# Performance work log

Hardware: AMD Instinct MI355X
Metric: run time of the kernel (lower is better)

Reference implementation:

```python
import jax, jax.numpy as jnp
import numpy as np


def setup_inputs() -> dict:
    key = jax.random.key(0)
    ks = jax.random.split(key, 4)
    B, S, D, E = 8, 4096, 2048, 64
    scale = 1.0 / np.sqrt(D)
    return {
        "x": jax.random.normal(ks[0], (B, S, D), dtype=jnp.float32),
        "W_route": jax.random.normal(ks[1], (E, D), dtype=jnp.float32) * scale,
        "b_route": jnp.zeros((E,), dtype=jnp.float32),
        "W_noise": jax.random.normal(ks[2], (E, D), dtype=jnp.float32) * scale,
        "b_noise": jnp.zeros((E,), dtype=jnp.float32),
        "noise_eps": jax.random.normal(ks[3], (B, S, E), dtype=jnp.float32),
    }


TOP_K = 2


def reference(x, W_route, b_route, W_noise, b_noise, noise_eps):
    # Dual linear projections: [B,S,D] @ [D,E] -> [B,S,E]
    logits = jnp.einsum("bsd,ed->bse", x, W_route) + b_route
    noise_logits = jnp.einsum("bsd,ed->bse", x, W_noise) + b_noise
    noisy_logits = logits + noise_eps * jax.nn.softplus(noise_logits)

    B, S, E = noisy_logits.shape
    flat = noisy_logits.reshape(B * S, E)
    top_vals, top_idx = jax.lax.top_k(flat, TOP_K)  # [N,K]

    # Scatter top-k values into -inf background, then softmax over experts.
    neg_inf = jnp.full_like(flat, -jnp.inf)
    rows = jnp.arange(B * S)[:, None]
    sparse = neg_inf.at[rows, top_idx].set(top_vals)
    router_output = jax.nn.softmax(sparse, axis=-1).reshape(B, S, E)
    indices = top_idx.reshape(B, S, TOP_K)
    return router_output, indices
```

## Files before the change

### kernel.cpp

```cpp
#include <hip/hip_runtime.h>
#include <math.h>

typedef _Float16 f16;
typedef __attribute__((ext_vector_type(8))) _Float16 half8;
typedef __attribute__((ext_vector_type(4))) float f32x4;

#define NEXP 64
#define TMR 32
#define TM 64
#define L_STRIDE 132

__device__ __forceinline__ float softplus_f(float x) {
    return fmaxf(x, 0.0f) + log1pf(expf(-fabsf(x)));
}

__device__ __forceinline__ void lds_dma16(const void* g, void* l) {
    __builtin_amdgcn_global_load_lds(
        (const __attribute__((address_space(1))) unsigned int*)g,
        (__attribute__((address_space(3))) unsigned int*)l, 16, 0, 0);
}

__device__ __forceinline__ void cvt_split(const float4 a, const float4 b,
                                          half8& hv, half8& lv) {
    const float vv[8] = {a.x, a.y, a.z, a.w, b.x, b.y, b.z, b.w};
#pragma unroll
    for (int j = 0; j < 8; ++j) {
        const f16 h = (f16)vv[j];
        hv[j] = h;
        lv[j] = (f16)((vv[j] - (float)h) * 4096.0f);
    }
}

__global__ void wsplit_kernel(const float* __restrict__ Wr,
                              const float* __restrict__ Wn,
                              f16* __restrict__ ws, int D) {
    const int per_col = D >> 3;
    const int t = blockIdx.x * blockDim.x + threadIdx.x;
    const int col = t / per_col;
    const int k0  = (t - col * per_col) * 8;
    if (col >= 128) return;
    const float* src = (col < NEXP) ? &Wr[(size_t)col * D] : &Wn[(size_t)(col - NEXP) * D];
    const float4 v0 = *(const float4*)&src[k0];
    const float4 v1 = *(const float4*)&src[k0 + 4];
    half8 hi, lo;
    cvt_split(v0, v1, hi, lo);
    const int kc = k0 >> 5, q = (k0 >> 3) & 3;
    const size_t base = (size_t)kc * 8192 + (size_t)q * 1024 + (size_t)col * 8;
    *(half8*)&ws[base]        = hi;
    *(half8*)&ws[base + 4096] = lo;
}

__global__ __launch_bounds__(256, 4)
void router_mfma_kernel(const float* __restrict__ x,
                        const f16* __restrict__ wsW,
                        const float* __restrict__ br,
                        const float* __restrict__ bn,
                        const float* __restrict__ eps,
                        float* __restrict__ out,
                        int N, int D) {
    __shared__ union alignas(16) {
        f16 B[2][8192];
        struct {
            float L[TMR][L_STRIDE];
            float p1[TMR], p2[TMR];
            int   i1[TMR], i2[TMR];
        } ep;
    } sm;

    const int tid  = threadIdx.x;
    const int lane = tid & 63;
    const int w    = tid >> 6;
    const int rowbase = blockIdx.x * TMR;
    const int wr = w & 1, wc = w >> 1;
    const int quad = lane >> 4;
    const int l16  = lane & 15;

    f32x4 accM[4], accC[4];
#pragma unroll
    for (int j = 0; j < 4; ++j) {
        accM[j] = (f32x4){0.f, 0.f, 0.f, 0.f};
        accC[j] = (f32x4){0.f, 0.f, 0.f, 0.f};
    }

    const float* xA = x + (size_t)(rowbase + wr * 16 + l16) * D + quad * 8;
    const int nkc = D >> 5;

    float4 aE0, aE1, aO0, aO1;

    {
        const char* gsrc = (const char*)wsW + w * 4096 + lane * 16;
        char* ldst = (char*)&sm.B[0][0] + w * 4096;
#pragma unroll
        for (int i = 0; i < 4; ++i) lds_dma16(gsrc + i * 1024, ldst + i * 1024);
        __builtin_amdgcn_sched_barrier(0);
        aE0 = *(const float4*)&xA[0];
        aE1 = *(const float4*)&xA[4];
        aO0 = *(const float4*)&xA[32];
        aO1 = *(const float4*)&xA[36];
        __builtin_amdgcn_sched_barrier(0);
        asm volatile("s_waitcnt vmcnt(4)" : : : "memory");
        __builtin_amdgcn_s_barrier();
        __builtin_amdgcn_sched_barrier(0);
    }

#define KLOOP_BODY(KC, A0, A1)                                                 \
    {                                                                          \
        const int cur = (KC) & 1, nxt = cur ^ 1;                               \
        if ((KC) + 1 < nkc) {                                                  \
            const char* gsrc = (const char*)wsW + (size_t)((KC) + 1) * 16384   \
                               + w * 4096 + lane * 16;                         \
            char* ldst = (char*)&sm.B[nxt][0] + w * 4096;                      \
            lds_dma16(gsrc,        ldst);                                      \
            lds_dma16(gsrc + 1024, ldst + 1024);                               \
            lds_dma16(gsrc + 2048, ldst + 2048);                               \
            lds_dma16(gsrc + 3072, ldst + 3072);                               \
        }                                                                      \
        __builtin_amdgcn_sched_barrier(0);                                     \
        half8 ah, al;                                                          \
        cvt_split(A0, A1, ah, al);                                             \
        if ((KC) + 2 < nkc) {                                                  \
            A0 = *(const float4*)&xA[((KC) + 2) * 32];                         \
            A1 = *(const float4*)&xA[((KC) + 2) * 32 + 4];                     \
        }                                                                      \
        __builtin_amdgcn_sched_barrier(0);                                     \
        half8 bh[4], bl[4];                                                    \
        _Pragma("unroll")                                                      \
        for (int ct = 0; ct < 4; ++ct) {                                       \
            const int c = (wc * 64 + ct * 16 + l16) * 8;                       \
            bh[ct] = *(const half8*)&sm.B[cur][quad * 1024 + c];               \
            bl[ct] = *(const half8*)&sm.B[cur][4096 + quad * 1024 + c];        \
        }                                                                      \
        _Pragma("unroll")                                                      \
        for (int ct = 0; ct < 4; ++ct) {                                       \
            accM[ct] = __builtin_amdgcn_mfma_f32_16x16x32_f16(                 \
                ah, bh[ct], accM[ct], 0, 0, 0);                                \
            accC[ct] = __builtin_amdgcn_mfma_f32_16x16x32_f16(                 \
                al, bh[ct], accC[ct], 0, 0, 0);                                \
            accC[ct] = __builtin_amdgcn_mfma_f32_16x16x32_f16(                 \
                ah, bl[ct], accC[ct], 0, 0, 0);                                \
        }                                                                      \
        if ((KC) + 2 < nkc)                                                    \
            asm volatile("s_waitcnt vmcnt(2) lgkmcnt(0)" : : : "memory");      \
        else                                                                   \
            asm volatile("s_waitcnt vmcnt(0) lgkmcnt(0)" : : : "memory");      \
        __builtin_amdgcn_s_barrier();                                          \
        __builtin_amdgcn_sched_barrier(0);                                     \
    }

    for (int kc = 0; kc < nkc; kc += 2) {
        KLOOP_BODY(kc,     aE0, aE1)
        KLOOP_BODY(kc + 1, aO0, aO1)
    }
#undef KLOOP_BODY

    {
        const float* bias = wc ? bn : br;
        const int row = wr * 16 + quad * 4;
#pragma unroll
        for (int ct = 0; ct < 4; ++ct) {
            const int col = wc * 64 + ct * 16 + l16;
            const float bcol = bias[ct * 16 + l16];
#pragma unroll
            for (int rg = 0; rg < 4; ++rg)
                sm.ep.L[row + rg][col] =
                    accM[ct][rg] + accC[ct][rg] * (1.0f / 4096.0f) + bcol;
        }
    }
    __syncthreads();

#pragma unroll
    for (int t = 0; t < 2; ++t) {
        const int f   = tid * 4 + t * 1024;
        const int row = f >> 6;
        const int e0  = f & 63;
        const float4 ev = *(const float4*)&eps[(size_t)(rowbase + row) * NEXP + e0];
        const float evs[4] = {ev.x, ev.y, ev.z, ev.w};
#pragma unroll
        for (int j = 0; j < 4; ++j) {
            const float lg = sm.ep.L[row][e0 + j];
            const float nz = sm.ep.L[row][NEXP + e0 + j];
            sm.ep.L[row][e0 + j] = fmaf(evs[j], softplus_f(nz), lg);
        }
    }
    __syncthreads();

    if (tid < TMR) {
        const int r = tid;
        float v1t = -INFINITY, v2t = -INFINITY;
        int i1 = 0, i2 = 0;
#pragma unroll 8
        for (int e = 0; e < NEXP; ++e) {
            const float v = sm.ep.L[r][e];
            if (v > v1t) { v2t = v1t; i2 = i1; v1t = v; i1 = e; }
            else if (v > v2t) { v2t = v; i2 = e; }
        }
        const float z = expf(v2t - v1t);
        const float s = 1.0f + z;
        sm.ep.p1[r] = 1.0f / s;
        sm.ep.p2[r] = z / s;
        sm.ep.i1[r] = i1;
        sm.ep.i2[r] = i2;
        float* oidx = out + (size_t)N * NEXP + (size_t)(rowbase + r) * 2;
        oidx[0] = (float)i1;
        oidx[1] = (float)i2;
    }
    __syncthreads();

    {
        const int r = tid >> 3;
        const int g = tid & 7;
        const float pa = sm.ep.p1[r], pb = sm.ep.p2[r];
        const int i1 = sm.ep.i1[r], i2 = sm.ep.i2[r];
        float* orow = out + (size_t)(rowbase + r) * NEXP;
#pragma unroll
        for (int t = 0; t < 2; ++t) {
            const int e0 = g * 8 + t * 4;
            float4 o;
            o.x = (e0 + 0 == i1) ? pa : ((e0 + 0 == i2) ? pb : 0.0f);
            o.y = (e0 + 1 == i1) ? pa : ((e0 + 1 == i2) ? pb : 0.0f);
            o.z = (e0 + 2 == i1) ? pa : ((e0 + 2 == i2) ? pb : 0.0f);
            o.w = (e0 + 3 == i1) ? pa : ((e0 + 3 == i2) ? pb : 0.0f);
            *(float4*)&orow[e0] = o;
        }
    }
}

#define BK 32
#define XS_STRIDE (TM + 4)
#define WS_STRIDE (128 + 4)

__global__ __launch_bounds__(256, 2)
void noisy_topk_router_kernel(const float* __restrict__ x,
                              const float* __restrict__ Wr,
                              const float* __restrict__ br,
                              const float* __restrict__ Wn,
                              const float* __restrict__ bn,
                              const float* __restrict__ eps,
                              float* __restrict__ out,
                              int N, int D) {
    __shared__ union alignas(16) {
        struct {
            float Xs[BK][XS_STRIDE];
            float Ws[BK][WS_STRIDE];
        } st;
        float L[TM][L_STRIDE];
    } sm;
    __shared__ float p1s[TM], p2s[TM];
    __shared__ int   i1s[TM], i2s[TM];

    const int tid = threadIdx.x;
    const int rowbase = blockIdx.x * TM;
    const int r0 = (tid >> 5) * 8;
    const int c0 = (tid & 31) * 4;

    float acc[8][4];
#pragma unroll
    for (int i = 0; i < 8; ++i)
#pragma unroll
        for (int j = 0; j < 4; ++j) acc[i][j] = 0.0f;

    const int q  = tid & 7;
    const int rr = tid >> 3;

    for (int k0 = 0; k0 < D; k0 += BK) {
#pragma unroll
        for (int i = 0; i < 2; ++i) {
            const int row = rr + 32 * i;
            const float4 xv = *(const float4*)&x[(size_t)(rowbase + row) * D + k0 + q * 4];
            sm.st.Xs[q * 4 + 0][row] = xv.x;
            sm.st.Xs[q * 4 + 1][row] = xv.y;
            sm.st.Xs[q * 4 + 2][row] = xv.z;
            sm.st.Xs[q * 4 + 3][row] = xv.w;
            const float4 wv = *(const float4*)&Wr[(size_t)row * D + k0 + q * 4];
            sm.st.Ws[q * 4 + 0][row] = wv.x;
            sm.st.Ws[q * 4 + 1][row] = wv.y;
            sm.st.Ws[q * 4 + 2][row] = wv.z;
            sm.st.Ws[q * 4 + 3][row] = wv.w;
            const float4 nv = *(const float4*)&Wn[(size_t)row * D + k0 + q * 4];
            sm.st.Ws[q * 4 + 0][NEXP + row] = nv.x;
            sm.st.Ws[q * 4 + 1][NEXP + row] = nv.y;
            sm.st.Ws[q * 4 + 2][NEXP + row] = nv.z;
            sm.st.Ws[q * 4 + 3][NEXP + row] = nv.w;
        }
        __syncthreads();
#pragma unroll 4
        for (int kk = 0; kk < BK; ++kk) {
            const float4 xa = *(const float4*)&sm.st.Xs[kk][r0];
            const float4 xb = *(const float4*)&sm.st.Xs[kk][r0 + 4];
            const float4 wv = *(const float4*)&sm.st.Ws[kk][c0];
            const float xs[8] = {xa.x, xa.y, xa.z, xa.w, xb.x, xb.y, xb.z, xb.w};
            const float ws[4] = {wv.x, wv.y, wv.z, wv.w};
#pragma unroll
            for (int i = 0; i < 8; ++i)
#pragma unroll
                for (int j = 0; j < 4; ++j)
                    acc[i][j] = fmaf(xs[i], ws[j], acc[i][j]);
        }
        __syncthreads();
    }
    {
        const float4 bv = (c0 < NEXP) ? *(const float4*)&br[c0]
                                      : *(const float4*)&bn[c0 - NEXP];
#pragma unroll
        for (int i = 0; i < 8; ++i) {
            float4 o;
            o.x = acc[i][0] + bv.x;
            o.y = acc[i][1] + bv.y;
            o.z = acc[i][2] + bv.z;
            o.w = acc[i][3] + bv.w;
            *(float4*)&sm.L[r0 + i][c0] = o;
        }
    }
    __syncthreads();
#pragma unroll
    for (int t = 0; t < 4; ++t) {
        const int f   = tid * 4 + t * 1024;
        const int row = f >> 6;
        const int e0  = f & 63;
        const float4 ev = *(const float4*)&eps[(size_t)(rowbase + row) * NEXP + e0];
        const float evs[4] = {ev.x, ev.y, ev.z, ev.w};
#pragma unroll
        for (int j = 0; j < 4; ++j) {
            const float lg = sm.L[row][e0 + j];
            const float nz = sm.L[row][NEXP + e0 + j];
            sm.L[row][e0 + j] = fmaf(evs[j], softplus_f(nz), lg);
        }
    }
    __syncthreads();
    if (tid < TM) {
        const int r = tid;
        float v1 = -INFINITY, v2 = -INFINITY;
        int i1 = 0, i2 = 0;
#pragma unroll 8
        for (int e = 0; e < NEXP; ++e) {
            const float v = sm.L[r][e];
            if (v > v1) { v2 = v1; i2 = i1; v1 = v; i1 = e; }
            else if (v > v2) { v2 = v; i2 = e; }
        }
        const float z = expf(v2 - v1);
        const float s = 1.0f + z;
        p1s[r] = 1.0f / s;
        p2s[r] = z / s;
        i1s[r] = i1;
        i2s[r] = i2;
        float* oidx = out + (size_t)N * NEXP + (size_t)(rowbase + r) * 2;
        oidx[0] = (float)i1;
        oidx[1] = (float)i2;
    }
    __syncthreads();
    {
        const int r = tid >> 2;
        const int g = tid & 3;
        const float pa = p1s[r], pb = p2s[r];
        const int i1 = i1s[r], i2 = i2s[r];
        float* orow = out + (size_t)(rowbase + r) * NEXP;
#pragma unroll
        for (int t = 0; t < 4; ++t) {
            const int e0 = g * 16 + t * 4;
            float4 o;
            o.x = (e0 + 0 == i1) ? pa : ((e0 + 0 == i2) ? pb : 0.0f);
            o.y = (e0 + 1 == i1) ? pa : ((e0 + 1 == i2) ? pb : 0.0f);
            o.z = (e0 + 2 == i1) ? pa : ((e0 + 2 == i2) ? pb : 0.0f);
            o.w = (e0 + 3 == i1) ? pa : ((e0 + 3 == i2) ? pb : 0.0f);
            *(float4*)&orow[e0] = o;
        }
    }
}

extern "C" void kernel_launch(void* const* d_in, const int* in_sizes, int n_in,
                              void* d_out, int out_size, void* d_ws, size_t ws_size,
                              hipStream_t stream) {
    const float* x   = (const float*)d_in[0];
    const float* Wr  = (const float*)d_in[1];
    const float* br  = (const float*)d_in[2];
    const float* Wn  = (const float*)d_in[3];
    const float* bn  = (const float*)d_in[4];
    const float* eps = (const float*)d_in[5];
    float* out = (float*)d_out;

    const int E = in_sizes[2];
    const int D = in_sizes[1] / E;
    const int N = in_sizes[0] / D;

    const size_t ws_needed = (size_t)128 * D * 2 * sizeof(f16);
    const bool fast = (E == 64) && (D == 2048) && (N % TMR == 0) && (ws_size >= ws_needed);

    if (fast) {
        const int pre_threads = 128 * (D / 8);
        wsplit_kernel<<<(pre_threads + 255) / 256, 256, 0, stream>>>(Wr, Wn, (f16*)d_ws, D);
        router_mfma_kernel<<<N / TMR, 256, 0, stream>>>(x, (const f16*)d_ws, br, bn, eps, out, N, D);
    } else {
        noisy_topk_router_kernel<<<N / TM, 256, 0, stream>>>(x, Wr, br, Wn, bn, eps, out, N, D);
    }
}
```

Before: 433.5 us.

## Load weight fragments directly to registers and shuffle x fragments instead of LDS staging

```diff
diff --git a/kernel.cpp b/kernel.cpp
--- a/kernel.cpp
+++ b/kernel.cpp
@@ -4,6 +4,7 @@
 typedef _Float16 f16;
 typedef __attribute__((ext_vector_type(8))) _Float16 half8;
 typedef __attribute__((ext_vector_type(4))) float f32x4;
+typedef __attribute__((ext_vector_type(4))) int i32x4;
 
 #define NEXP 64
 #define TMR 32
@@ -14,12 +15,6 @@
     return fmaxf(x, 0.0f) + log1pf(expf(-fabsf(x)));
 }
 
-__device__ __forceinline__ void lds_dma16(const void* g, void* l) {
-    __builtin_amdgcn_global_load_lds(
-        (const __attribute__((address_space(1))) unsigned int*)g,
-        (__attribute__((address_space(3))) unsigned int*)l, 16, 0, 0);
-}
-
 __device__ __forceinline__ void cvt_split(const float4 a, const float4 b,
                                           half8& hv, half8& lv) {
     const float vv[8] = {a.x, a.y, a.z, a.w, b.x, b.y, b.z, b.w};
@@ -29,6 +24,14 @@
         hv[j] = h;
         lv[j] = (f16)((vv[j] - (float)h) * 4096.0f);
     }
+}
+
+__device__ __forceinline__ half8 shfl_frag(half8 v, int s) {
+    union { half8 h; i32x4 i; } u;
+    u.h = v;
+#pragma unroll
+    for (int j = 0; j < 4; ++j) u.i[j] = __shfl(u.i[j], s, 64);
+    return u.h;
 }
 
 __global__ void wsplit_kernel(const float* __restrict__ Wr,
@@ -50,7 +53,7 @@
     *(half8*)&ws[base + 4096] = lo;
 }
 
-__global__ __launch_bounds__(256, 4)
+__global__ __launch_bounds__(256, 2)
 void router_mfma_kernel(const float* __restrict__ x,
                         const f16* __restrict__ wsW,
                         const float* __restrict__ br,
@@ -58,14 +61,11 @@
                         const float* __restrict__ eps,
                         float* __restrict__ out,
                         int N, int D) {
-    __shared__ union alignas(16) {
-        f16 B[2][8192];
-        struct {
-            float L[TMR][L_STRIDE];
-            float p1[TMR], p2[TMR];
-            int   i1[TMR], i2[TMR];
-        } ep;
-    } sm;
+    __shared__ struct {
+        float L[TMR][L_STRIDE];
+        float p1[TMR], p2[TMR];
+        int   i1[TMR], i2[TMR];
+    } ep;
 
     const int tid  = threadIdx.x;
     const int lane = tid & 63;
@@ -74,6 +74,7 @@
     const int wr = w & 1, wc = w >> 1;
     const int quad = lane >> 4;
     const int l16  = lane & 15;
+    const int shsrc = (l16 << 2) | quad;
 
     f32x4 accM[4], accC[4];
 #pragma unroll
@@ -82,76 +83,79 @@
         accC[j] = (f32x4){0.f, 0.f, 0.f, 0.f};
     }
 
-    const float* xA = x + (size_t)(rowbase + wr * 16 + l16) * D + quad * 8;
+    const float* xp = x + (size_t)(rowbase + wr * 16 + (lane >> 2)) * D + (lane & 3) * 8;
+    const f16* wsB = wsW + quad * 1024 + (size_t)(wc * 64 + l16) * 8;
+
     const int nkc = D >> 5;
 
-    float4 aE0, aE1, aO0, aO1;
-
-    {
-        const char* gsrc = (const char*)wsW + w * 4096 + lane * 16;
-        char* ldst = (char*)&sm.B[0][0] + w * 4096;
-#pragma unroll
-        for (int i = 0; i < 4; ++i) lds_dma16(gsrc + i * 1024, ldst + i * 1024);
-        __builtin_amdgcn_sched_barrier(0);
-        aE0 = *(const float4*)&xA[0];
-        aE1 = *(const float4*)&xA[4];
-        aO0 = *(const float4*)&xA[32];
-        aO1 = *(const float4*)&xA[36];
-        __builtin_amdgcn_sched_barrier(0);
-        asm volatile("s_waitcnt vmcnt(4)" : : : "memory");
-        __builtin_amdgcn_s_barrier();
-        __builtin_amdgcn_sched_barrier(0);
-    }
-
-#define KLOOP_BODY(KC, A0, A1)                                                 \
+    float4 xE0 = *(const float4*)&xp[0];
+    float4 xE1 = *(const float4*)&xp[4];
+    float4 xO0 = *(const float4*)&xp[32];
+    float4 xO1 = *(const float4*)&xp[36];
+    __builtin_amdgcn_sched_barrier(0);
+    half8 bE0 = *(const half8*)&wsB[0];
+    half8 bE1 = *(const half8*)&wsB[128];
+    half8 bE2 = *(const half8*)&wsB[256];
+    half8 bE3 = *(const half8*)&wsB[384];
+    half8 bE4 = *(const half8*)&wsB[4096];
+    half8 bE5 = *(const half8*)&wsB[4224];
+    half8 bE6 = *(const half8*)&wsB[4352];
+    half8 bE7 = *(const half8*)&wsB[4480];
+    half8 bO0 = *(const half8*)&wsB[8192];
+    half8 bO1 = *(const half8*)&wsB[8192 + 128];
+    half8 bO2 = *(const half8*)&wsB[8192 + 256];
+    half8 bO3 = *(const half8*)&wsB[8192 + 384];
+    half8 bO4 = *(const half8*)&wsB[8192 + 4096];
+    half8 bO5 = *(const half8*)&wsB[8192 + 4224];
+    half8 bO6 = *(const half8*)&wsB[8192 + 4352];
+    half8 bO7 = *(const half8*)&wsB[8192 + 4480];
+    __builtin_amdgcn_sched_barrier(0);
+
+#define KBODY(KC, XA0, XA1, B0, B1, B2, B3, B4, B5, B6, B7)                    \
     {                                                                          \
-        const int cur = (KC) & 1, nxt = cur ^ 1;                               \
-        if ((KC) + 1 < nkc) {                                                  \
-            const char* gsrc = (const char*)wsW + (size_t)((KC) + 1) * 16384   \
-                               + w * 4096 + lane * 16;                         \
-            char* ldst = (char*)&sm.B[nxt][0] + w * 4096;                      \
-            lds_dma16(gsrc,        ldst);                                      \
-            lds_dma16(gsrc + 1024, ldst + 1024);                               \
-            lds_dma16(gsrc + 2048, ldst + 2048);                               \
-            lds_dma16(gsrc + 3072, ldst + 3072);                               \
+        half8 hv, lv;                                                          \
+        cvt_split(XA0, XA1, hv, lv);             \
+        __builtin_amdgcn_sched_barrier(0);                                     \
+        if ((KC) + 2 < nkc) {                 \
+            XA0 = *(const float4*)&xp[((KC) + 2) * 32];                        \
+            XA1 = *(const float4*)&xp[((KC) + 2) * 32 + 4];                    \
         }                                                                      \
         __builtin_amdgcn_sched_barrier(0);                                     \
-        half8 ah, al;                                                          \
-        cvt_split(A0, A1, ah, al);                                             \
-        if ((KC) + 2 < nkc) {                                                  \
-            A0 = *(const float4*)&xA[((KC) + 2) * 32];                         \
-            A1 = *(const float4*)&xA[((KC) + 2) * 32 + 4];                     \
+        const half8 ah = shfl_frag(hv, shsrc);                                 \
+        const half8 al = shfl_frag(lv, shsrc);                                 \
+        __builtin_amdgcn_sched_barrier(0);                                     \
+        accM[0] = __builtin_amdgcn_mfma_f32_16x16x32_f16(ah, B0, accM[0], 0, 0, 0); \
+        accC[0] = __builtin_amdgcn_mfma_f32_16x16x32_f16(al, B0, accC[0], 0, 0, 0); \
+        accC[0] = __builtin_amdgcn_mfma_f32_16x16x32_f16(ah, B4, accC[0], 0, 0, 0); \
+        accM[1] = __builtin_amdgcn_mfma_f32_16x16x32_f16(ah, B1, accM[1], 0, 0, 0); \
+        accC[1] = __builtin_amdgcn_mfma_f32_16x16x32_f16(al, B1, accC[1], 0, 0, 0); \
+        accC[1] = __builtin_amdgcn_mfma_f32_16x16x32_f16(ah, B5, accC[1], 0, 0, 0); \
+        accM[2] = __builtin_amdgcn_mfma_f32_16x16x32_f16(ah, B2, accM[2], 0, 0, 0); \
+        accC[2] = __builtin_amdgcn_mfma_f32_16x16x32_f16(al, B2, accC[2], 0, 0, 0); \
+        accC[2] = __builtin_amdgcn_mfma_f32_16x16x32_f16(ah, B6, accC[2], 0, 0, 0); \
+        accM[3] = __builtin_amdgcn_mfma_f32_16x16x32_f16(ah, B3, accM[3], 0, 0, 0); \
+        accC[3] = __builtin_amdgcn_mfma_f32_16x16x32_f16(al, B3, accC[3], 0, 0, 0); \
+        accC[3] = __builtin_amdgcn_mfma_f32_16x16x32_f16(ah, B7, accC[3], 0, 0, 0); \
+        __builtin_amdgcn_sched_barrier(0);                                     \
+        if ((KC) + 2 < nkc) {                      \
+            const f16* bp = wsB + (size_t)((KC) + 2) * 8192;                   \
+            B0 = *(const half8*)&bp[0];                                        \
+            B1 = *(const half8*)&bp[128];                                      \
+            B2 = *(const half8*)&bp[256];                                      \
+            B3 = *(const half8*)&bp[384];                                      \
+            B4 = *(const half8*)&bp[4096];                                     \
+            B5 = *(const half8*)&bp[4224];                                     \
+            B6 = *(const half8*)&bp[4352];                                     \
+            B7 = *(const half8*)&bp[4480];                                     \
         }                                                                      \
         __builtin_amdgcn_sched_barrier(0);                                     \
-        half8 bh[4], bl[4];                                                    \
-        _Pragma("unroll")                                                      \
-        for (int ct = 0; ct < 4; ++ct) {                                       \
-            const int c = (wc * 64 + ct * 16 + l16) * 8;                       \
-            bh[ct] = *(const half8*)&sm.B[cur][quad * 1024 + c];               \
-            bl[ct] = *(const half8*)&sm.B[cur][4096 + quad * 1024 + c];        \
-        }                                                                      \
-        _Pragma("unroll")                                                      \
-        for (int ct = 0; ct < 4; ++ct) {                                       \
-            accM[ct] = __builtin_amdgcn_mfma_f32_16x16x32_f16(                 \
-                ah, bh[ct], accM[ct], 0, 0, 0);                                \
-            accC[ct] = __builtin_amdgcn_mfma_f32_16x16x32_f16(                 \
-                al, bh[ct], accC[ct], 0, 0, 0);                                \
-            accC[ct] = __builtin_amdgcn_mfma_f32_16x16x32_f16(                 \
-                ah, bl[ct], accC[ct], 0, 0, 0);                                \
-        }                                                                      \
-        if ((KC) + 2 < nkc)                                                    \
-            asm volatile("s_waitcnt vmcnt(2) lgkmcnt(0)" : : : "memory");      \
-        else                                                                   \
-            asm volatile("s_waitcnt vmcnt(0) lgkmcnt(0)" : : : "memory");      \
-        __builtin_amdgcn_s_barrier();                                          \
-        __builtin_amdgcn_sched_barrier(0);                                     \
     }
 
     for (int kc = 0; kc < nkc; kc += 2) {
-        KLOOP_BODY(kc,     aE0, aE1)
-        KLOOP_BODY(kc + 1, aO0, aO1)
-    }
-#undef KLOOP_BODY
+        KBODY(kc,     xE0, xE1, bE0, bE1, bE2, bE3, bE4, bE5, bE6, bE7)
+        KBODY(kc + 1, xO0, xO1, bO0, bO1, bO2, bO3, bO4, bO5, bO6, bO7)
+    }
+#undef KBODY
 
     {
         const float* bias = wc ? bn : br;
@@ -162,7 +166,7 @@
             const float bcol = bias[ct * 16 + l16];
 #pragma unroll
             for (int rg = 0; rg < 4; ++rg)
-                sm.ep.L[row + rg][col] =
+                ep.L[row + rg][col] =
                     accM[ct][rg] + accC[ct][rg] * (1.0f / 4096.0f) + bcol;
         }
     }
@@ -177,9 +181,9 @@
         const float evs[4] = {ev.x, ev.y, ev.z, ev.w};
 #pragma unroll
         for (int j = 0; j < 4; ++j) {
-            const float lg = sm.ep.L[row][e0 + j];
-            const float nz = sm.ep.L[row][NEXP + e0 + j];
-            sm.ep.L[row][e0 + j] = fmaf(evs[j], softplus_f(nz), lg);
+            const float lg = ep.L[row][e0 + j];
+            const float nz = ep.L[row][NEXP + e0 + j];
+            ep.L[row][e0 + j] = fmaf(evs[j], softplus_f(nz), lg);
         }
     }
     __syncthreads();
@@ -190,16 +194,16 @@
         int i1 = 0, i2 = 0;
 #pragma unroll 8
         for (int e = 0; e < NEXP; ++e) {
-            const float v = sm.ep.L[r][e];
+            const float v = ep.L[r][e];
             if (v > v1t) { v2t = v1t; i2 = i1; v1t = v; i1 = e; }
             else if (v > v2t) { v2t = v; i2 = e; }
         }
         const float z = expf(v2t - v1t);
         const float s = 1.0f + z;
-        sm.ep.p1[r] = 1.0f / s;
-        sm.ep.p2[r] = z / s;
-        sm.ep.i1[r] = i1;
-        sm.ep.i2[r] = i2;
+        ep.p1[r] = 1.0f / s;
+        ep.p2[r] = z / s;
+        ep.i1[r] = i1;
+        ep.i2[r] = i2;
         float* oidx = out + (size_t)N * NEXP + (size_t)(rowbase + r) * 2;
         oidx[0] = (float)i1;
         oidx[1] = (float)i2;
@@ -209,8 +213,8 @@
     {
         const int r = tid >> 3;
         const int g = tid & 7;
-        const float pa = sm.ep.p1[r], pb = sm.ep.p2[r];
-        const int i1 = sm.ep.i1[r], i2 = sm.ep.i2[r];
+        const float pa = ep.p1[r], pb = ep.p2[r];
+        const int i1 = ep.i1[r], i2 = ep.i2[r];
         float* orow = out + (size_t)(rowbase + r) * NEXP;
 #pragma unroll
         for (int t = 0; t < 2; ++t) {
```

Result: slower. 463.8 us (+7.0%).
